# Optimization experiments

Hardware: AMD Instinct MI355X
Metric: run time of the kernel (lower is better)

## Reference

```python
import jax, jax.numpy as jnp
import numpy as np

NV, NS = 100000, 50000
EVV, EH, EIN, ESS = 1_600_000, 800_000, 800_000, 800_000
DIN, H, OUT, K, NREL = 5, 64, 8, 3, 3


def _seg_sum(x, idx, n):
    return jax.ops.segment_sum(x, idx, num_segments=n)


def _seg_mean(x, idx, n):
    s = _seg_sum(x, idx, n)
    c = _seg_sum(jnp.ones(idx.shape, x.dtype), idx, n)
    return s / jnp.maximum(c, 1.0)[:, None]


def rgcn(x, ei, etype, W_rel, W_root, b):
    # PyG RGCNConv: per-relation mean aggregation + root transform + bias
    src, dst = ei[0], ei[1]
    out = x @ W_root + b
    for r in range(NREL):
        xr = x @ W_rel[r]                    # [NV,H] transform-then-gather
        w = (etype == r).astype(x.dtype)     # [E] relation mask
        s = _seg_sum(xr[src] * w[:, None], dst, NV)
        c = _seg_sum(w, dst, NV)
        out = out + s / jnp.maximum(c, 1.0)[:, None]
    return out


def tag(x, ei, W, b, n):
    # PyG TAGConv: sym-normalized (no self loops) K-hop propagation, per-hop linear
    src, dst = ei[0], ei[1]
    deg = _seg_sum(jnp.ones(src.shape, x.dtype), dst, n)
    dinv = jnp.where(deg > 0, jax.lax.rsqrt(jnp.maximum(deg, 1.0)), 0.0)
    norm = dinv[src] * dinv[dst]             # [E]
    out = x @ W[0]
    h = x
    for k in range(1, K + 1):
        h = _seg_sum(norm[:, None] * h[src], dst, n)
        out = out + h @ W[k]
    return out + b


def graph_conv(x_src, x_dst, ei, ew, W_rel, b, W_root, n_dst):
    # PyG GraphConv (aggr='add'): lin_rel(sum_j w_ij x_j) + lin_root(x_i)
    src, dst = ei[0], ei[1]
    agg = _seg_sum(ew[:, None] * x_src[src], dst, n_dst)
    return agg @ W_rel + b + x_dst @ W_root


def sage(x_src, x_dst, ei, W_l, b, W_r, n_dst):
    # PyG SAGEConv (aggr='mean'): lin_l(mean_j x_j) + lin_r(x_i)
    src, dst = ei[0], ei[1]
    agg = _seg_mean(x_src[src], dst, n_dst)
    return agg @ W_l + b + x_dst @ W_r


def setup_inputs() -> dict:
    key = jax.random.key(0)
    ks = jax.random.split(key, 40)
    f32 = jnp.float32

    def nrm(k, shape, fan_in):
        return jax.random.normal(k, shape, f32) / np.sqrt(fan_in)

    def ei(k, e, nsrc, ndst):
        k1, k2 = jax.random.split(k)
        return jnp.stack([jax.random.randint(k1, (e,), 0, nsrc),
                          jax.random.randint(k2, (e,), 0, ndst)]).astype(jnp.int64)

    inp = {
        'game_x': jax.random.normal(ks[0], (NV, DIN), f32),
        'state_x': jax.random.normal(ks[1], (NS, DIN), f32),
        'edge_index_v_v': ei(ks[2], EVV, NV, NV),
        'edge_type_v_v': jax.random.randint(ks[3], (EVV,), 0, NREL).astype(jnp.int64),
        'edge_index_history_v_s': ei(ks[4], EH, NV, NS),
        'edge_attr_history_v_s': jax.random.uniform(ks[5], (EH,), f32),
        'edge_index_in_v_s': ei(ks[6], EIN, NV, NS),
        'edge_index_s_s': ei(ks[7], ESS, NS, NS),
        # conv1 RGCN(5,H,3)
        'W1_rel': nrm(ks[8], (NREL, DIN, H), DIN), 'W1_root': nrm(ks[9], (DIN, H), DIN), 'b1': jnp.zeros((H,), f32),
        # conv12 TAG(5,H,K=3)
        'W12': nrm(ks[10], (K + 1, DIN, H), DIN), 'b12': jnp.zeros((H,), f32),
        # conv2 TAG(H,H,K=3)
        'W2': nrm(ks[11], (K + 1, H, H), H), 'b2': jnp.zeros((H,), f32),
        # conv3 GraphConv((H,DIN)->H)
        'W3_rel': nrm(ks[12], (H, H), H), 'W3_root': nrm(ks[13], (DIN, H), DIN), 'b3': jnp.zeros((H,), f32),
        # conv32 SAGE((H,H)->H)
        'W32_l': nrm(ks[14], (H, H), H), 'W32_r': nrm(ks[15], (H, H), H), 'b32': jnp.zeros((H,), f32),
        'W4_l': nrm(ks[16], (H, H), H), 'W4_r': nrm(ks[17], (H, H), H), 'b4': jnp.zeros((H,), f32),
        'W42_l': nrm(ks[18], (H, H), H), 'W42_r': nrm(ks[19], (H, H), H), 'b42': jnp.zeros((H,), f32),
        'W5_l': nrm(ks[20], (H, H), H), 'W5_r': nrm(ks[21], (H, H), H), 'b5': jnp.zeros((H,), f32),
        'Wl': nrm(ks[22], (H, OUT), H), 'bl': jnp.zeros((OUT,), f32),
    }
    return inp


def reference(game_x, state_x, edge_index_v_v, edge_type_v_v,
              edge_index_history_v_s, edge_attr_history_v_s,
              edge_index_in_v_s, edge_index_s_s,
              W1_rel, W1_root, b1, W12, b12, W2, b2,
              W3_rel, W3_root, b3, W32_l, W32_r, b32,
              W4_l, W4_r, b4, W42_l, W42_r, b42,
              W5_l, W5_r, b5, Wl, bl):
    gx = rgcn(game_x, edge_index_v_v, edge_type_v_v, W1_rel, W1_root, b1) \
        + tag(game_x, edge_index_v_v, W12, b12, NV)          # group(..., 'sum')
    sx = jax.nn.relu(graph_conv(gx, state_x, edge_index_history_v_s,
                                edge_attr_history_v_s, W3_rel, b3, W3_root, NS))
    sx = jax.nn.relu(sage(gx, sx, edge_index_history_v_s, W32_l, b32, W32_r, NS))
    sx = jax.nn.relu(sage(gx, sx, edge_index_in_v_s, W4_l, b4, W4_r, NS))
    sx = jax.nn.relu(sage(gx, sx, edge_index_in_v_s, W42_l, b42, W42_r, NS))
    sx = jax.nn.relu(tag(sx, edge_index_s_s, W2, b2, NS))
    sx = jax.nn.relu(sage(sx, sx, edge_index_s_s, W5_l, b5, W5_r, NS))
    return sx @ Wl + bl
```

## Files before the change

kernel.cpp:

```cpp
#include <hip/hip_runtime.h>

#define NVV 100000
#define NSV 50000
#define E_VV 1600000
#define E_H  800000
#define E_IN 800000
#define E_SS 800000
#define ETOT 4000000
#define DIN 5
#define H_ROW 100000
#define IN_ROW 150000
#define SS_ROW 200000
#define NROWS 250000
#define POS_H  E_VV
#define POS_IN (E_VV + E_H)
#define POS_SS (E_VV + E_H + E_IN)
#define NBUK 196
#define NBUKS 98
#define NBTOT 490
#define BUK_H  196
#define BUK_IN 294
#define BUK_SS 392
#define BSHIFT 9
#define T1 4096
#define TC 16384
#define G1VV 391
#define G1S  196
#define SB1  (G1VV + 3 * G1S)

__device__ __forceinline__ unsigned short f2bf(float x) {
  unsigned b = __float_as_uint(x);
  return (unsigned short)((b + 0x7FFFu + ((b >> 16) & 1u)) >> 16);
}
__device__ __forceinline__ float bf2f(unsigned short u) {
  return __uint_as_float(((unsigned)u) << 16);
}


__global__ __launch_bounds__(256)
void k_bucket_count(const int* __restrict__ d_vv, const int* __restrict__ d_h,
                    const int* __restrict__ d_in, const int* __restrict__ d_ss,
                    int* __restrict__ bcnt) {
  __shared__ int h[NBTOT];
  const int tid = threadIdx.x;
  for (int i = tid; i < NBTOT; i += 256) h[i] = 0;
  __syncthreads();
  const int base = blockIdx.x * TC;
#pragma unroll 4
  for (int k = 0; k < TC / 256; k++) {
    int e = base + k * 256 + tid;
    int bi = -1;
    if (e < E_VV) bi = d_vv[e] >> BSHIFT;
    else if (e < POS_IN) bi = BUK_H + (d_h[e - POS_H] >> BSHIFT);
    else if (e < POS_SS) bi = BUK_IN + (d_in[e - POS_IN] >> BSHIFT);
    else if (e < ETOT) bi = BUK_SS + (d_ss[e - POS_SS] >> BSHIFT);
    if (bi >= 0) atomicAdd(&h[bi], 1);
  }
  __syncthreads();
  for (int i = tid; i < NBTOT; i += 256) if (h[i]) atomicAdd(&bcnt[i], h[i]);
}

__global__ __launch_bounds__(512)
void k_bucket_scan(const int* __restrict__ bcnt, int* __restrict__ bbase, int* __restrict__ cb) {
  __shared__ int sd[512];
  int t = threadIdx.x;
  int v = (t < NBTOT) ? bcnt[t] : 0;
  sd[t] = v; __syncthreads();
  for (int off = 1; off < 512; off <<= 1) {
    int x = (t >= off) ? sd[t - off] : 0;
    __syncthreads();
    sd[t] += x;
    __syncthreads();
  }
  int segstart = (t < BUK_H) ? 0 : (t < BUK_IN) ? BUK_H : (t < BUK_SS) ? BUK_IN : BUK_SS;
  int excl = ((t > 0) ? sd[t - 1] : 0) - ((segstart > 0) ? sd[segstart - 1] : 0);
  if (t < NBTOT) { bbase[t] = excl; cb[t] = excl; }
}

__global__ __launch_bounds__(256)
void k_fill_s1_all(const int* __restrict__ s_vv, const int* __restrict__ d_vv,
                   const int* __restrict__ et,
                   const int* __restrict__ s_h, const int* __restrict__ d_h,
                   const float* __restrict__ ew,
                   const int* __restrict__ s_in, const int* __restrict__ d_in,
                   const int* __restrict__ s_ss, const int* __restrict__ d_ss,
                   int* __restrict__ cb,
                   unsigned* __restrict__ temp_vv, uint2* __restrict__ temp_h,
                   unsigned* __restrict__ temp_in, unsigned* __restrict__ temp_ss) {
  __shared__ int hist[NBUK], lbase[NBUK], run[NBUK], gb[NBUK];
  __shared__ int sc[256];
  __shared__ unsigned stage[T1];
  __shared__ unsigned stageW[T1];
  __shared__ int gpos[T1];
  const int tid = threadIdx.x;
  const int b = blockIdx.x;
  int g, tile;
  if (b < G1VV) { g = 0; tile = b; }
  else if (b < G1VV + G1S) { g = 1; tile = b - G1VV; }
  else if (b < G1VV + 2 * G1S) { g = 2; tile = b - G1VV - G1S; }
  else { g = 3; tile = b - G1VV - 2 * G1S; }
  const int ne = (g == 0) ? E_VV : E_H;
  const int nbuk = (g == 0) ? NBUK : NBUKS;
  const int cboff = (g == 0) ? 0 : (g == 1) ? BUK_H : (g == 2) ? BUK_IN : BUK_SS;
  const int* S = (g == 0) ? s_vv : (g == 1) ? s_h : (g == 2) ? s_in : s_ss;
  const int* D = (g == 0) ? d_vv : (g == 1) ? d_h : (g == 2) ? d_in : d_ss;
  const int base = tile * T1;
  const int nvalid = min(T1, ne - base);
  for (int i = tid; i < nbuk; i += 256) { hist[i] = 0; run[i] = 0; }
  __syncthreads();
  int dv[16]; unsigned pk[16], pkw[16];
#pragma unroll
  for (int k = 0; k < 16; k++) {
    int e = base + k * 256 + tid;
    if (e - base < nvalid) {
      int d = D[e];
      dv[k] = d;
      if (g == 0) pk[k] = (unsigned)(((d & 511) << 19) | (et[e] << 17) | S[e]);
      else pk[k] = (unsigned)(((d & 511) << 17) | S[e]);
      if (g == 1) pkw[k] = (unsigned)__float_as_int(ew[e]);
      atomicAdd(&hist[d >> BSHIFT], 1);
    } else dv[k] = -1;
  }
  __syncthreads();
  int my = (tid < nbuk) ? hist[tid] : 0;
  sc[tid] = my; __syncthreads();
  for (int off = 1; off < 256; off <<= 1) {
    int t = (tid >= off) ? sc[tid - off] : 0;
    __syncthreads();
    sc[tid] += t;
    __syncthreads();
  }
  if (tid < nbuk) {
    lbase[tid] = sc[tid] - my;
    gb[tid] = my ? atomicAdd(&cb[cboff + tid], my) : 0;
  }
  __syncthreads();
#pragma unroll
  for (int k = 0; k < 16; k++) {
    if (dv[k] >= 0) {
      int bu = dv[k] >> BSHIFT;
      int loc = atomicAdd(&run[bu], 1);
      int li = lbase[bu] + loc;
      stage[li] = pk[k];
      if (g == 1) stageW[li] = pkw[k];
      gpos[li] = gb[bu] + loc;
    }
  }
  __syncthreads();
  if (g == 0)      for (int i = tid; i < nvalid; i += 256) temp_vv[gpos[i]] = stage[i];
  else if (g == 1) for (int i = tid; i < nvalid; i += 256) temp_h[gpos[i]] = make_uint2(stage[i], stageW[i]);
  else if (g == 2) for (int i = tid; i < nvalid; i += 256) temp_in[gpos[i]] = stage[i];
  else             for (int i = tid; i < nvalid; i += 256) temp_ss[gpos[i]] = stage[i];
}

__global__ __launch_bounds__(256)
void k_fill_s2_all(const unsigned* __restrict__ temp_vv, const uint2* __restrict__ temp_h,
                   const unsigned* __restrict__ temp_in, const unsigned* __restrict__ temp_ss,
                   const int* __restrict__ bbase,
                   unsigned* __restrict__ payload_vv, int2* __restrict__ eh,
                   int* __restrict__ srcs_in, int* __restrict__ srcs_ss,
                   int* __restrict__ rs_all, int* __restrict__ cnt_all,
                   const float* __restrict__ x, float4* __restrict__ xp,
                   float* __restrict__ dinvS) {
  __shared__ int lcnt[512], lpos[512];
  __shared__ int sc[256];
  const int b = blockIdx.x, tid = threadIdx.x;
  int g, lb;
  if (b < BUK_H) { g = 0; lb = b; }
  else if (b < BUK_IN) { g = 1; lb = b - BUK_H; }
  else if (b < BUK_SS) { g = 2; lb = b - BUK_IN; }
  else { g = 3; lb = b - BUK_SS; }
  const int d0 = lb << BSHIFT;
  const int nrows = (g == 0) ? NVV : NSV;
  const int rowbase = (g == 0) ? 0 : (g == 1) ? H_ROW : (g == 2) ? IN_ROW : SS_ROW;
  const int ne = (g == 0) ? E_VV : E_H;
  const int lastb = (g == 0) ? NBUK - 1 : NBUKS - 1;
  const int shift = (g == 0) ? 19 : 17;
  lcnt[tid] = 0; lcnt[tid + 256] = 0;
  __syncthreads();
  const int gstart = bbase[b];
  const int gend = (lb == lastb) ? ne : bbase[b + 1];
  if (g == 1) {
    for (int i = gstart + tid; i < gend; i += 256) atomicAdd(&lcnt[temp_h[i].x >> 17], 1);
  } else {
    const unsigned* tp = (g == 0) ? temp_vv : (g == 2) ? temp_in : temp_ss;
    for (int i = gstart + tid; i < gend; i += 256) atomicAdd(&lcnt[tp[i] >> shift], 1);
  }
  __syncthreads();
  int c0 = lcnt[2 * tid], c1 = lcnt[2 * tid + 1];
  int ps = c0 + c1;
  sc[tid] = ps; __syncthreads();
  for (int off = 1; off < 256; off <<= 1) {
    int x2 = (tid >= off) ? sc[tid - off] : 0;
    __syncthreads();
    sc[tid] += x2;
    __syncthreads();
  }
  int basep = gstart + sc[tid] - ps;
  lpos[2 * tid] = basep;
  lpos[2 * tid + 1] = basep + c0;
  __syncthreads();
  for (int d = tid; d < 512; d += 256) {
    int gd = d0 + d;
    if (gd < nrows) {
      rs_all[rowbase + gd] = lpos[d];
      cnt_all[rowbase + gd] = lcnt[d];
      if (g == 0) {
        float dc = (float)lcnt[d];
        float di = dc > 0.f ? rsqrtf(dc) : 0.f;
        const float* xr = x + (size_t)gd * 5;
        xp[gd * 2]     = make_float4(xr[0], xr[1], xr[2], xr[3]);
        xp[gd * 2 + 1] = make_float4(xr[4], di, 0.f, 0.f);
      } else if (g == 3) {
        float dc = (float)lcnt[d];
        dinvS[gd] = dc > 0.f ? rsqrtf(dc) : 0.f;
      }
    }
  }
  __syncthreads();
  if (g == 0) {
    for (int i = gstart + tid; i < gend; i += 256) {
      unsigned en = temp_vv[i];
      int pos = atomicAdd(&lpos[en >> 19], 1);
      payload_vv[pos] = en & 0x7FFFFu;
    }
  } else if (g == 1) {
    for (int i = gstart + tid; i < gend; i += 256) {
      uint2 en = temp_h[i];
      int pos = atomicAdd(&lpos[en.x >> 17], 1);
      eh[pos] = make_int2((int)(en.x & 0x1FFFFu), (int)en.y);
    }
  } else if (g == 2) {
    for (int i = gstart + tid; i < gend; i += 256) {
      unsigned en = temp_in[i];
      int pos = atomicAdd(&lpos[en >> 17], 1);
      srcs_in[pos] = (int)(en & 0x1FFFFu);
    }
  } else {
    for (int i = gstart + tid; i < gend; i += 256) {
      unsigned en = temp_ss[i];
      int pos = atomicAdd(&lpos[en >> 17], 1);
      srcs_ss[pos] = (int)(en & 0x1FFFFu);
    }
  }
}


__global__ __launch_bounds__(256)
void k_vv_pass1(const float4* __restrict__ xp,
                const int* __restrict__ rowstart, const int* __restrict__ cnt,
                const unsigned* __restrict__ payload,
                float4* __restrict__ ra4all, float4* __restrict__ h1p) {
  int d = blockIdx.x * 256 + threadIdx.x;
  if (d >= NVV) return;
  int rs = rowstart[d], c = cnt[d];
  float a0[5] = {0,0,0,0,0}, a1[5] = {0,0,0,0,0}, a2[5] = {0,0,0,0,0}, h[5] = {0,0,0,0,0};
  float c0 = 0.f, c1 = 0.f, c2 = 0.f;
  int j = 0;
  for (; j + 2 <= c; j += 2) {
    unsigned pA = payload[rs + j], pB = payload[rs + j + 1];
    int sA = pA & 0x1FFFF, rA = pA >> 17;
    int sB = pB & 0x1FFFF, rB = pB >> 17;
    float4 xA0 = xp[sA * 2], xA1 = xp[sA * 2 + 1];
    float4 xB0 = xp[sB * 2], xB1 = xp[sB * 2 + 1];
    float xsA[5] = {xA0.x, xA0.y, xA0.z, xA0.w, xA1.x};
    float xsB[5] = {xB0.x, xB0.y, xB0.z, xB0.w, xB1.x};
    float wA = xA1.y, wB = xB1.y;
    float mA0 = (rA == 0) ? 1.f : 0.f, mA1 = (rA == 1) ? 1.f : 0.f, mA2 = (rA == 2) ? 1.f : 0.f;
    float mB0 = (rB == 0) ? 1.f : 0.f, mB1 = (rB == 1) ? 1.f : 0.f, mB2 = (rB == 2) ? 1.f : 0.f;
    c0 += mA0 + mB0; c1 += mA1 + mB1; c2 += mA2 + mB2;
#pragma unroll
    for (int k = 0; k < 5; k++) {
      h[k] += wA * xsA[k] + wB * xsB[k];
      a0[k] += mA0 * xsA[k] + mB0 * xsB[k];
      a1[k] += mA1 * xsA[k] + mB1 * xsB[k];
      a2[k] += mA2 * xsA[k] + mB2 * xsB[k];
    }
  }
  for (; j < c; j++) {
    unsigned p = payload[rs + j];
    int s = p & 0x1FFFF, r = p >> 17;
    float4 x0 = xp[s * 2], x1 = xp[s * 2 + 1];
    float xs[5] = {x0.x, x0.y, x0.z, x0.w, x1.x};
    float wsc = x1.y;
    float m0 = (r == 0) ? 1.f : 0.f, m1 = (r == 1) ? 1.f : 0.f, m2 = (r == 2) ? 1.f : 0.f;
    c0 += m0; c1 += m1; c2 += m2;
#pragma unroll
    for (int k = 0; k < 5; k++) {
      h[k] += wsc * xs[k];
      a0[k] += m0 * xs[k]; a1[k] += m1 * xs[k]; a2[k] += m2 * xs[k];
    }
  }
  float dv = xp[d * 2 + 1].y;
  float4* ra4 = ra4all + d * 5;
  ra4[0] = make_float4(a0[0], a0[1], a0[2], a0[3]);
  ra4[1] = make_float4(a0[4], a1[0], a1[1], a1[2]);
  ra4[2] = make_float4(a1[3], a1[4], a2[0], a2[1]);
  ra4[3] = make_float4(a2[2], a2[3], a2[4], c0);
  ra4[4] = make_float4(c1, c2, 0.f, 0.f);
  h1p[d * 2]     = make_float4(dv * h[0], dv * h[1], dv * h[2], dv * h[3]);
  h1p[d * 2 + 1] = make_float4(dv * h[4], dv, 0.f, 0.f);
}

__global__ __launch_bounds__(256)
void k_vv_hop(const float4* __restrict__ hinp,
              const int* __restrict__ rowstart, const int* __restrict__ cnt,
              const unsigned* __restrict__ payload, float4* __restrict__ houtp) {
  int d = blockIdx.x * 256 + threadIdx.x;
  if (d >= NVV) return;
  int rs = rowstart[d], c = cnt[d];
  float h[5] = {0,0,0,0,0};
  int j = 0;
  for (; j + 4 <= c; j += 4) {
    unsigned p0 = payload[rs + j], p1 = payload[rs + j + 1];
    unsigned p2 = payload[rs + j + 2], p3 = payload[rs + j + 3];
    int s0 = p0 & 0x1FFFF, s1 = p1 & 0x1FFFF, s2 = p2 & 0x1FFFF, s3 = p3 & 0x1FFFF;
    float4 a0 = hinp[s0 * 2], b0 = hinp[s0 * 2 + 1];
    float4 a1 = hinp[s1 * 2], b1 = hinp[s1 * 2 + 1];
    float4 a2 = hinp[s2 * 2], b2 = hinp[s2 * 2 + 1];
    float4 a3 = hinp[s3 * 2], b3 = hinp[s3 * 2 + 1];
    float w0 = b0.y, w1 = b1.y, w2 = b2.y, w3 = b3.y;
    h[0] += w0 * a0.x + w1 * a1.x + w2 * a2.x + w3 * a3.x;
    h[1] += w0 * a0.y + w1 * a1.y + w2 * a2.y + w3 * a3.y;
    h[2] += w0 * a0.z + w1 * a1.z + w2 * a2.z + w3 * a3.z;
    h[3] += w0 * a0.w + w1 * a1.w + w2 * a2.w + w3 * a3.w;
    h[4] += w0 * b0.x + w1 * b1.x + w2 * b2.x + w3 * b3.x;
  }
  for (; j < c; j++) {
    int s = payload[rs + j] & 0x1FFFF;
    float4 x0 = hinp[s * 2], x1 = hinp[s * 2 + 1];
    float wsc = x1.y;
    h[0] += wsc * x0.x; h[1] += wsc * x0.y; h[2] += wsc * x0.z; h[3] += wsc * x0.w;
    h[4] += wsc * x1.x;
  }
  float dv = hinp[d * 2 + 1].y;
  houtp[d * 2]     = make_float4(dv * h[0], dv * h[1], dv * h[2], dv * h[3]);
  houtp[d * 2 + 1] = make_float4(dv * h[4], dv, 0.f, 0.f);
}

__global__ __launch_bounds__(256)
void k_combine_gx(const float4* __restrict__ xp,
                  const float4* __restrict__ ra4all,
                  const float4* __restrict__ h1p, const float4* __restrict__ h2p,
                  const float4* __restrict__ h3p,
                  const float* __restrict__ W1_rel, const float* __restrict__ W1_root,
                  const float* __restrict__ b1,
                  const float* __restrict__ W12, const float* __restrict__ b12,
                  unsigned short* __restrict__ gx16) {
  __shared__ float Ws[7 * 320];
  __shared__ float bs[64];
  int tid = threadIdx.x;
  for (int i = tid; i < 320; i += 256) {
    Ws[i]        = W1_root[i] + W12[i];
    Ws[320 + i]  = W1_rel[i];
    Ws[640 + i]  = W1_rel[320 + i];
    Ws[960 + i]  = W1_rel[640 + i];
    Ws[1280 + i] = W12[320 + i];
    Ws[1600 + i] = W12[640 + i];
    Ws[1920 + i] = W12[960 + i];
  }
  if (tid < 64) bs[tid] = b1[tid] + b12[tid];
  __syncthreads();
  const int f = tid & 63;
  const int grp = tid >> 6;
  float wcol[35];
#pragma unroll
  for (int t = 0; t < 35; t++) wcol[t] = Ws[t * 64 + f];
  const float bias = bs[f];
  const int v0 = blockIdx.x * 32 + grp * 8;
  for (int n = 0; n < 8; n++) {
    int v = v0 + n;
    if (v >= NVV) return;
    float in[35];
    {
      float4 x0 = xp[v * 2], x1 = xp[v * 2 + 1];
      in[0] = x0.x; in[1] = x0.y; in[2] = x0.z; in[3] = x0.w; in[4] = x1.x;
    }
    {
      const float4* ra = ra4all + v * 5;
      float4 r0 = ra[0], r1 = ra[1], r2 = ra[2], r3 = ra[3], r4 = ra[4];
      float i0 = 1.0f / fmaxf(r3.w, 1.0f);
      float i1 = 1.0f / fmaxf(r4.x, 1.0f);
      float i2 = 1.0f / fmaxf(r4.y, 1.0f);
      in[5]  = r0.x * i0; in[6]  = r0.y * i0; in[7]  = r0.z * i0; in[8]  = r0.w * i0; in[9]  = r1.x * i0;
      in[10] = r1.y * i1; in[11] = r1.z * i1; in[12] = r1.w * i1; in[13] = r2.x * i1; in[14] = r2.y * i1;
      in[15] = r2.z * i2; in[16] = r2.w * i2; in[17] = r3.x * i2; in[18] = r3.y * i2; in[19] = r3.z * i2;
    }
    {
      float4 a = h1p[v * 2], b = h1p[v * 2 + 1];
      in[20] = a.x; in[21] = a.y; in[22] = a.z; in[23] = a.w; in[24] = b.x;
      a = h2p[v * 2]; b = h2p[v * 2 + 1];
      in[25] = a.x; in[26] = a.y; in[27] = a.z; in[28] = a.w; in[29] = b.x;
      a = h3p[v * 2]; b = h3p[v * 2 + 1];
      in[30] = a.x; in[31] = a.y; in[32] = a.z; in[33] = a.w; in[34] = b.x;
    }
    float acc = bias;
#pragma unroll
    for (int t = 0; t < 35; t++) acc += in[t] * wcol[t];
    gx16[v * 64 + f] = f2bf(acc);
  }
}


__global__ __launch_bounds__(256)
void k_aggB(const unsigned short* __restrict__ X16,
            const int* __restrict__ rs_h, const int* __restrict__ cnt_h,
            const int2* __restrict__ eh,
            const int* __restrict__ rs_in, const int* __restrict__ cnt_in,
            const int* __restrict__ srcs_in,
            float* __restrict__ outw, float* __restrict__ outu, float* __restrict__ outIN,
            int nb64) {
  int bb = blockIdx.x;
  int lane = threadIdx.x & 63;
  if (bb < nb64) {
    int wid = bb * 4 + (threadIdx.x >> 6);
    if (wid >= NSV) return;
    int rs = rs_h[wid], c = cnt_h[wid];
    float aw = 0.f, au = 0.f;
    int j = 0;
    for (; j + 8 <= c; j += 8) {
      int2 p0 = eh[rs + j],     p1 = eh[rs + j + 1], p2 = eh[rs + j + 2], p3 = eh[rs + j + 3];
      int2 p4 = eh[rs + j + 4], p5 = eh[rs + j + 5], p6 = eh[rs + j + 6], p7 = eh[rs + j + 7];
      float v0 = bf2f(X16[p0.x * 64 + lane]);
      float v1 = bf2f(X16[p1.x * 64 + lane]);
      float v2 = bf2f(X16[p2.x * 64 + lane]);
      float v3 = bf2f(X16[p3.x * 64 + lane]);
      float v4 = bf2f(X16[p4.x * 64 + lane]);
      float v5 = bf2f(X16[p5.x * 64 + lane]);
      float v6 = bf2f(X16[p6.x * 64 + lane]);
      float v7 = bf2f(X16[p7.x * 64 + lane]);
      au += ((v0 + v1) + (v2 + v3)) + ((v4 + v5) + (v6 + v7));
      aw += __int_as_float(p0.y) * v0 + __int_as_float(p1.y) * v1
          + __int_as_float(p2.y) * v2 + __int_as_float(p3.y) * v3
          + __int_as_float(p4.y) * v4 + __int_as_float(p5.y) * v5
          + __int_as_float(p6.y) * v6 + __int_as_float(p7.y) * v7;
    }
    for (; j < c; j++) {
      int2 p = eh[rs + j];
      float v = bf2f(X16[p.x * 64 + lane]);
      au += v; aw += __int_as_float(p.y) * v;
    }
    outw[wid * 64 + lane] = aw;
    outu[wid * 64 + lane] = au;
  } else {
    int wid = (bb - nb64) * 4 + (threadIdx.x >> 6);
    if (wid >= NSV) return;
    int rs = rs_in[wid], c = cnt_in[wid];
    float a = 0.f;
    int j = 0;
    for (; j + 8 <= c; j += 8) {
      int s0 = srcs_in[rs + j],     s1 = srcs_in[rs + j + 1], s2 = srcs_in[rs + j + 2], s3 = srcs_in[rs + j + 3];
      int s4 = srcs_in[rs + j + 4], s5 = srcs_in[rs + j + 5], s6 = srcs_in[rs + j + 6], s7 = srcs_in[rs + j + 7];
      float v0 = bf2f(X16[s0 * 64 + lane]);
      float v1 = bf2f(X16[s1 * 64 + lane]);
      float v2 = bf2f(X16[s2 * 64 + lane]);
      float v3 = bf2f(X16[s3 * 64 + lane]);
      float v4 = bf2f(X16[s4 * 64 + lane]);
      float v5 = bf2f(X16[s5 * 64 + lane]);
      float v6 = bf2f(X16[s6 * 64 + lane]);
      float v7 = bf2f(X16[s7 * 64 + lane]);
      a += ((v0 + v1) + (v2 + v3)) + ((v4 + v5) + (v6 + v7));
    }
    for (; j < c; j++) a += bf2f(X16[srcs_in[rs + j] * 64 + lane]);
    outIN[wid * 64 + lane] = a;
  }
}

__global__ __launch_bounds__(256)
void k_agg64b(const unsigned short* __restrict__ X16,
              const int* __restrict__ rowstart, const int* __restrict__ cnt,
              const int* __restrict__ srcs, float* __restrict__ out, int n) {
  int wid = blockIdx.x * 4 + (threadIdx.x >> 6);
  if (wid >= n) return;
  int lane = threadIdx.x & 63;
  int rs = rowstart[wid], c = cnt[wid];
  float a = 0.f;
  int j = 0;
  for (; j + 8 <= c; j += 8) {
    int s0 = srcs[rs + j],     s1 = srcs[rs + j + 1], s2 = srcs[rs + j + 2], s3 = srcs[rs + j + 3];
    int s4 = srcs[rs + j + 4], s5 = srcs[rs + j + 5], s6 = srcs[rs + j + 6], s7 = srcs[rs + j + 7];
    float v0 = bf2f(X16[s0 * 64 + lane]);
    float v1 = bf2f(X16[s1 * 64 + lane]);
    float v2 = bf2f(X16[s2 * 64 + lane]);
    float v3 = bf2f(X16[s3 * 64 + lane]);
    float v4 = bf2f(X16[s4 * 64 + lane]);
    float v5 = bf2f(X16[s5 * 64 + lane]);
    float v6 = bf2f(X16[s6 * 64 + lane]);
    float v7 = bf2f(X16[s7 * 64 + lane]);
    a += ((v0 + v1) + (v2 + v3)) + ((v4 + v5) + (v6 + v7));
  }
  for (; j < c; j++) a += bf2f(X16[srcs[rs + j] * 64 + lane]);
  out[wid * 64 + lane] = a;
}

__global__ __launch_bounds__(256)
void k_tag64b(const unsigned short* __restrict__ U16,
              const int* __restrict__ rowstart, const int* __restrict__ cnt,
              const int* __restrict__ srcs, const float* __restrict__ dinv,
              unsigned short* __restrict__ t_out, unsigned short* __restrict__ u_out, int n) {
  int wid = blockIdx.x * 4 + (threadIdx.x >> 6);
  if (wid >= n) return;
  int lane = threadIdx.x & 63;
  int rs = rowstart[wid], c = cnt[wid];
  float a = 0.f;
  int j = 0;
  for (; j + 8 <= c; j += 8) {
    int s0 = srcs[rs + j],     s1 = srcs[rs + j + 1], s2 = srcs[rs + j + 2], s3 = srcs[rs + j + 3];
    int s4 = srcs[rs + j + 4], s5 = srcs[rs + j + 5], s6 = srcs[rs + j + 6], s7 = srcs[rs + j + 7];
    float v0 = bf2f(U16[s0 * 64 + lane]);
    float v1 = bf2f(U16[s1 * 64 + lane]);
    float v2 = bf2f(U16[s2 * 64 + lane]);
    float v3 = bf2f(U16[s3 * 64 + lane]);
    float v4 = bf2f(U16[s4 * 64 + lane]);
    float v5 = bf2f(U16[s5 * 64 + lane]);
    float v6 = bf2f(U16[s6 * 64 + lane]);
    float v7 = bf2f(U16[s7 * 64 + lane]);
    a += ((v0 + v1) + (v2 + v3)) + ((v4 + v5) + (v6 + v7));
  }
  for (; j < c; j++) a += bf2f(U16[srcs[rs + j] * 64 + lane]);
  float dv = dinv[wid];
  float t = dv * a;
  t_out[wid * 64 + lane] = f2bf(t);
  if (u_out) u_out[wid * 64 + lane] = f2bf(dv * t);
}


__device__ __forceinline__ void mm_zero(float acc[4][4]) {
#pragma unroll
  for (int j = 0; j < 4; j++)
#pragma unroll
    for (int jj = 0; jj < 4; jj++) acc[j][jj] = 0.f;
}

__device__ __forceinline__ void mm_acc(const float* sA, const float* sW, int K,
                                       int nl0, int f0, float acc[4][4]) {
  for (int k = 0; k < K; k++) {
    float4 w = *(const float4*)(&sW[k * 64 + f0]);
#pragma unroll
    for (int j = 0; j < 4; j++) {
      float a = sA[(nl0 + j) * 68 + k];
      acc[j][0] += a * w.x; acc[j][1] += a * w.y; acc[j][2] += a * w.z; acc[j][3] += a * w.w;
    }
  }
}

__device__ __forceinline__ void mm_loadw(float* Ws, const float* W, int tid) {
  const float4* w4 = (const float4*)W;
  float4* s4 = (float4*)Ws;
  for (int i = tid; i < 1024; i += 256) s4[i] = w4[i];
}

__device__ __forceinline__ void mm_stage_f32(float* as, const float* A, const int* cntA,
                                             int gb, int n, int tid) {
  for (int i = tid; i < 1024; i += 256) {
    int nl = i >> 4, k4 = i & 15;
    int g = gb + nl;
    float4 v = make_float4(0.f, 0.f, 0.f, 0.f);
    if (g < n) {
      v = ((const float4*)A)[g * 16 + k4];
      if (cntA) {
        float sc = 1.0f / fmaxf((float)cntA[g], 1.0f);
        v.x *= sc; v.y *= sc; v.z *= sc; v.w *= sc;
      }
    }
    *(float4*)(&as[nl * 68 + k4 * 4]) = v;
  }
}

__device__ __forceinline__ void mm_stage_bf16(float* as, const unsigned short* A,
                                              int gb, int n, int tid) {
  for (int i = tid; i < 1024; i += 256) {
    int nl = i >> 4, k4 = i & 15;
    int g = gb + nl;
    float4 v = make_float4(0.f, 0.f, 0.f, 0.f);
    if (g < n) {
      uint2 u = ((const uint2*)(A + (size_t)g * 64))[k4];
      v.x = bf2f((unsigned short)(u.x & 0xFFFF));
      v.y = bf2f((unsigned short)(u.x >> 16));
      v.z = bf2f((unsigned short)(u.y & 0xFFFF));
      v.w = bf2f((unsigned short)(u.y >> 16));
    }
    *(float4*)(&as[nl * 68 + k4 * 4]) = v;
  }
}

__global__ __launch_bounds__(256)
void k_mm_chainC(const float* __restrict__ aggHw, const float* __restrict__ state_x,
                 const float* __restrict__ aggHu, const int* __restrict__ cnt_h,
                 const float* __restrict__ aggIN, const int* __restrict__ cnt_in,
                 const float* __restrict__ W3_rel, const float* __restrict__ W3_root,
                 const float* __restrict__ b3,
                 const float* __restrict__ W32_l, const float* __restrict__ W32_r,
                 const float* __restrict__ b32,
                 const float* __restrict__ W4_l, const float* __restrict__ W4_r,
                 const float* __restrict__ b4,
                 const float* __restrict__ W42_l, const float* __restrict__ W42_r,
                 const float* __restrict__ b42,
                 float* __restrict__ S2out, unsigned short* __restrict__ S2b,
                 const float* __restrict__ dinvS, int n) {
  __shared__ float Ws[4096];
  __shared__ float as[64 * 68];
  __shared__ float cs[64 * 68];
  const int tid = threadIdx.x;
  const int gb = blockIdx.x * 64;
  const int lane = tid & 63;
  const int fq = lane & 15, nq = lane >> 4;
  const int f0 = fq * 4;
  const int nl0 = (tid >> 6) * 16 + nq * 4;
  float acc[4][4];

  mm_loadw(Ws, W3_rel, tid);
  mm_stage_f32(as, aggHw, nullptr, gb, n, tid);
  __syncthreads();
  mm_zero(acc);
  mm_acc(as, Ws, 64, nl0, f0, acc);
  __syncthreads();
  for (int i = tid; i < 320; i += 256) {
    int nl = i / 5, k = i - nl * 5;
    int g = gb + nl;
    as[nl * 68 + k] = (g < n) ? state_x[(size_t)g * 5 + k] : 0.f;
  }
  for (int i = tid; i < 320; i += 256) Ws[i] = W3_root[i];
  __syncthreads();
  mm_acc(as, Ws, 5, nl0, f0, acc);
#pragma unroll
  for (int j = 0; j < 4; j++)
#pragma unroll
    for (int jj = 0; jj < 4; jj++)
      cs[(nl0 + j) * 68 + f0 + jj] = fmaxf(acc[j][jj] + b3[f0 + jj], 0.f);
  __syncthreads();

  mm_loadw(Ws, W32_l, tid);
  mm_stage_f32(as, aggHu, cnt_h, gb, n, tid);
  __syncthreads();
  mm_zero(acc);
  mm_acc(as, Ws, 64, nl0, f0, acc);
  __syncthreads();
  mm_loadw(Ws, W32_r, tid);
  __syncthreads();
  mm_acc(cs, Ws, 64, nl0, f0, acc);
  __syncthreads();
#pragma unroll
  for (int j = 0; j < 4; j++)
#pragma unroll
    for (int jj = 0; jj < 4; jj++)
      cs[(nl0 + j) * 68 + f0 + jj] = fmaxf(acc[j][jj] + b32[f0 + jj], 0.f);
  __syncthreads();

  mm_loadw(Ws, W4_l, tid);
  mm_stage_f32(as, aggIN, cnt_in, gb, n, tid);
  __syncthreads();
  mm_zero(acc);
  mm_acc(as, Ws, 64, nl0, f0, acc);
  __syncthreads();
  mm_loadw(Ws, W4_r, tid);
  __syncthreads();
  mm_acc(cs, Ws, 64, nl0, f0, acc);
  __syncthreads();
#pragma unroll
  for (int j = 0; j < 4; j++)
#pragma unroll
    for (int jj = 0; jj < 4; jj++)
      cs[(nl0 + j) * 68 + f0 + jj] = fmaxf(acc[j][jj] + b4[f0 + jj], 0.f);
  __syncthreads();

  mm_loadw(Ws, W42_l, tid);
  mm_stage_f32(as, aggIN, cnt_in, gb, n, tid);
  __syncthreads();
  mm_zero(acc);
  mm_acc(as, Ws, 64, nl0, f0, acc);
  __syncthreads();
  mm_loadw(Ws, W42_r, tid);
  __syncthreads();
  mm_acc(cs, Ws, 64, nl0, f0, acc);
#pragma unroll
  for (int j = 0; j < 4; j++) {
    int g = gb + nl0 + j;
    if (g < n) {
      float osc = dinvS[g];
#pragma unroll
      for (int jj = 0; jj < 4; jj++) {
        int f = f0 + jj;
        float v = fmaxf(acc[j][jj] + b42[f], 0.f);
        S2out[(size_t)g * 64 + f] = v;
        S2b[(size_t)g * 64 + f] = f2bf(v * osc);
      }
    }
  }
}

__global__ __launch_bounds__(256)
void k_mm_d(const float* __restrict__ S2, const unsigned short* __restrict__ t1b,
            const unsigned short* __restrict__ t2b, const unsigned short* __restrict__ t3b,
            const float* __restrict__ W2, const float* __restrict__ b2,
            float* __restrict__ S1, unsigned short* __restrict__ S1b, int n) {
  __shared__ float Ws[4096];
  __shared__ float as[64 * 68];
  const int tid = threadIdx.x;
  const int gb = blockIdx.x * 64;
  const int lane = tid & 63;
  const int fq = lane & 15, nq = lane >> 4;
  const int f0 = fq * 4;
  const int nl0 = (tid >> 6) * 16 + nq * 4;
  float acc[4][4];
  mm_zero(acc);
  mm_loadw(Ws, W2, tid);
  mm_stage_f32(as, S2, nullptr, gb, n, tid);
  __syncthreads();
  mm_acc(as, Ws, 64, nl0, f0, acc);
  __syncthreads();
  mm_loadw(Ws, W2 + 4096, tid);
  mm_stage_bf16(as, t1b, gb, n, tid);
  __syncthreads();
  mm_acc(as, Ws, 64, nl0, f0, acc);
  __syncthreads();
  mm_loadw(Ws, W2 + 8192, tid);
  mm_stage_bf16(as, t2b, gb, n, tid);
  __syncthreads();
  mm_acc(as, Ws, 64, nl0, f0, acc);
  __syncthreads();
  mm_loadw(Ws, W2 + 12288, tid);
  mm_stage_bf16(as, t3b, gb, n, tid);
  __syncthreads();
  mm_acc(as, Ws, 64, nl0, f0, acc);
#pragma unroll
  for (int j = 0; j < 4; j++) {
    int g = gb + nl0 + j;
    if (g < n) {
#pragma unroll
      for (int jj = 0; jj < 4; jj++) {
        int f = f0 + jj;
        float v = fmaxf(acc[j][jj] + b2[f], 0.f);
        S1[(size_t)g * 64 + f] = v;
        S1b[(size_t)g * 64 + f] = f2bf(v);
      }
    }
  }
}

__global__ __launch_bounds__(256)
void k_mm_e(const float* __restrict__ aggSS, const int* __restrict__ cnt_ss,
            const float* __restrict__ W5_l, const float* __restrict__ S1,
            const float* __restrict__ W5_r, const float* __restrict__ b5,
            const float* __restrict__ Wl, const float* __restrict__ bl,
            float* __restrict__ out, int n) {
  __shared__ float Ws[4096];
  __shared__ float as[64 * 68];
  __shared__ float cs[64 * 68];
  const int tid = threadIdx.x;
  const int gb = blockIdx.x * 64;
  const int lane = tid & 63;
  const int fq = lane & 15, nq = lane >> 4;
  const int f0 = fq * 4;
  const int nl0 = (tid >> 6) * 16 + nq * 4;
  float acc[4][4];
  mm_zero(acc);
  mm_loadw(Ws, W5_l, tid);
  mm_stage_f32(as, aggSS, cnt_ss, gb, n, tid);
  __syncthreads();
  mm_acc(as, Ws, 64, nl0, f0, acc);
  __syncthreads();
  mm_loadw(Ws, W5_r, tid);
  mm_stage_f32(cs, S1, nullptr, gb, n, tid);
  __syncthreads();
  mm_acc(cs, Ws, 64, nl0, f0, acc);
  __syncthreads();
#pragma unroll
  for (int j = 0; j < 4; j++)
#pragma unroll
    for (int jj = 0; jj < 4; jj++)
      as[(nl0 + j) * 68 + f0 + jj] = fmaxf(acc[j][jj] + b5[f0 + jj], 0.f);
  for (int i = tid; i < 512; i += 256) Ws[i] = Wl[i];
  __syncthreads();
#pragma unroll
  for (int q = 0; q < 2; q++) {
    int idx = tid * 2 + q;
    int nl = idx >> 3, o = idx & 7;
    int g = gb + nl;
    if (g < n) {
      float a2 = bl[o];
#pragma unroll 8
      for (int k = 0; k < 64; k++) a2 += as[nl * 68 + k] * Ws[k * 8 + o];
      out[(size_t)g * 8 + o] = a2;
    }
  }
}


extern "C" void kernel_launch(void* const* d_in, const int* in_sizes, int n_in,
                              void* d_out, int out_size, void* d_ws, size_t ws_size,
                              hipStream_t stream) {
  const float* game_x  = (const float*)d_in[0];
  const float* state_x = (const float*)d_in[1];
  const int*   ei_vv   = (const int*)d_in[2];
  const int*   et_vv   = (const int*)d_in[3];
  const int*   ei_h    = (const int*)d_in[4];
  const float* ew_h    = (const float*)d_in[5];
  const int*   ei_in   = (const int*)d_in[6];
  const int*   ei_ss   = (const int*)d_in[7];
  const float* W1_rel  = (const float*)d_in[8];
  const float* W1_root = (const float*)d_in[9];
  const float* b1      = (const float*)d_in[10];
  const float* W12     = (const float*)d_in[11];
  const float* b12     = (const float*)d_in[12];
  const float* W2      = (const float*)d_in[13];
  const float* b2      = (const float*)d_in[14];
  const float* W3_rel  = (const float*)d_in[15];
  const float* W3_root = (const float*)d_in[16];
  const float* b3      = (const float*)d_in[17];
  const float* W32_l   = (const float*)d_in[18];
  const float* W32_r   = (const float*)d_in[19];
  const float* b32     = (const float*)d_in[20];
  const float* W4_l    = (const float*)d_in[21];
  const float* W4_r    = (const float*)d_in[22];
  const float* b4      = (const float*)d_in[23];
  const float* W42_l   = (const float*)d_in[24];
  const float* W42_r   = (const float*)d_in[25];
  const float* b42     = (const float*)d_in[26];
  const float* W5_l    = (const float*)d_in[27];
  const float* W5_r    = (const float*)d_in[28];
  const float* b5      = (const float*)d_in[29];
  const float* Wl      = (const float*)d_in[30];
  const float* bl      = (const float*)d_in[31];

  float* ws = (float*)d_ws;
  int*   cnt_all = (int*)(ws + 0);
  int*   rs_all  = (int*)(ws + 250000);
  int*   bcnt    = (int*)(ws + 500000);
  int*   bbase   = (int*)(ws + 500512);
  int*   cb      = (int*)(ws + 501024);
  int*   srcs_ss = (int*)(ws + 760000);
  float4* x_pad  = (float4*)(ws + 1600000);
  float4* h1p    = (float4*)(ws + 2400000);
  float4* h2p    = (float4*)(ws + 3200000);
  float4* h3p    = (float4*)(ws + 4000000);
  float4* ra4all = (float4*)(ws + 4800000);
  float* dinvS   = ws + 6800000;
  unsigned short* gx16 = (unsigned short*)(ws + 6850000);
  unsigned* temp_vv    = (unsigned*)(ws + 6850000);
  float* aggHw = ws + 10050000;
  float* aggHu = ws + 13250000;
  float* aggIN = ws + 16450000;
  float* S1    = ws + 19650000;
  float* S2    = ws + 22850000;
  uint2*    temp_h  = (uint2*)aggHw;
  unsigned* temp_in = (unsigned*)(aggHw + 1600000);
  unsigned* temp_ss = (unsigned*)(aggHw + 2400000);
  unsigned short* S2b = (unsigned short*)(ws + 4800000);
  unsigned short* u1b = (unsigned short*)(aggHw + 1600000);
  float*          aggSS = aggHw + 1600000;
  unsigned short* t1b = (unsigned short*)aggHu;
  unsigned short* t2b = (unsigned short*)(aggHu + 1600000);
  unsigned short* t3b = (unsigned short*)aggIN;
  unsigned short* S1b = (unsigned short*)(aggIN + 1600000);
  unsigned* payload_vv = (unsigned*)S1;
  unsigned short* u2b  = (unsigned short*)S1;
  int2*     eh         = (int2*)S2;
  int*      srcs_in    = (int*)(S2 + 1600000);

  const int* src_vv = ei_vv;  const int* dst_vv = ei_vv + E_VV;
  const int* src_h  = ei_h;   const int* dst_h  = ei_h + E_H;
  const int* src_in = ei_in;  const int* dst_in = ei_in + E_IN;
  const int* src_ss = ei_ss;  const int* dst_ss = ei_ss + E_SS;

  auto nblk = [](long long n) { return dim3((unsigned)((n + 255) / 256)); };
  const int NB64 = (NSV + 3) / 4;
  const int NB   = (NSV + 63) / 64;
  const int GC   = (ETOT + TC - 1) / TC;

  int* cnt_h  = cnt_all + H_ROW;
  int* cnt_in = cnt_all + IN_ROW;
  int* cnt_ss = cnt_all + SS_ROW;
  int* rs_vv  = rs_all;
  int* rs_h   = rs_all + H_ROW;
  int* rs_in  = rs_all + IN_ROW;
  int* rs_ss  = rs_all + SS_ROW;

  hipMemsetAsync(bcnt, 0, NBTOT * sizeof(int), stream);
  k_bucket_count<<<GC, 256, 0, stream>>>(dst_vv, dst_h, dst_in, dst_ss, bcnt);
  k_bucket_scan<<<1, 512, 0, stream>>>(bcnt, bbase, cb);
  k_fill_s1_all<<<SB1, 256, 0, stream>>>(src_vv, dst_vv, et_vv, src_h, dst_h, ew_h,
                                         src_in, dst_in, src_ss, dst_ss, cb,
                                         temp_vv, temp_h, temp_in, temp_ss);
  k_fill_s2_all<<<NBTOT, 256, 0, stream>>>(temp_vv, temp_h, temp_in, temp_ss, bbase,
                                           payload_vv, eh, srcs_in, srcs_ss,
                                           rs_all, cnt_all, game_x, x_pad, dinvS);

  k_vv_pass1<<<nblk(NVV), 256, 0, stream>>>(x_pad, rs_vv, cnt_all, payload_vv, ra4all, h1p);
  k_vv_hop<<<nblk(NVV), 256, 0, stream>>>(h1p, rs_vv, cnt_all, payload_vv, h2p);
  k_vv_hop<<<nblk(NVV), 256, 0, stream>>>(h2p, rs_vv, cnt_all, payload_vv, h3p);
  k_combine_gx<<<dim3((NVV + 31) / 32), 256, 0, stream>>>(x_pad, ra4all, h1p, h2p, h3p,
                                                          W1_rel, W1_root, b1, W12, b12, gx16);

  k_aggB<<<2 * NB64, 256, 0, stream>>>(gx16, rs_h, cnt_h, eh, rs_in, cnt_in, srcs_in,
                                       aggHw, aggHu, aggIN, NB64);

  k_mm_chainC<<<NB, 256, 0, stream>>>(aggHw, state_x, aggHu, cnt_h, aggIN, cnt_in,
                                      W3_rel, W3_root, b3, W32_l, W32_r, b32,
                                      W4_l, W4_r, b4, W42_l, W42_r, b42,
                                      S2, S2b, dinvS, NSV);

  k_tag64b<<<NB64, 256, 0, stream>>>(S2b, rs_ss, cnt_ss, srcs_ss, dinvS, t1b, u1b, NSV);
  k_tag64b<<<NB64, 256, 0, stream>>>(u1b, rs_ss, cnt_ss, srcs_ss, dinvS, t2b, u2b, NSV);
  k_tag64b<<<NB64, 256, 0, stream>>>(u2b, rs_ss, cnt_ss, srcs_ss, dinvS, t3b, nullptr, NSV);
  k_mm_d<<<NB, 256, 0, stream>>>(S2, t1b, t2b, t3b, W2, b2, S1, S1b, NSV);

  k_agg64b<<<NB64, 256, 0, stream>>>(S1b, rs_ss, cnt_ss, srcs_ss, aggSS, NSV);
  k_mm_e<<<NB, 256, 0, stream>>>(aggSS, cnt_ss, W5_l, S1, W5_r, b5, Wl, bl, (float*)d_out, NSV);
}
```

Before: 683.4 us.

## Software-pipeline weight and activation loads into registers in dense matmul kernels

Splits the shared-memory staging of weights and activation tiles into a register issue phase and a commit phase. The next stage's global loads are issued before the current matmul runs, so their latency overlaps compute. Biases, root weights, state features and dinv scales are also hoisted into registers at kernel start. This removes one barrier per layer, but raises register pressure from the extra float4 buffers, which could lower occupancy.

```diff
diff --git a/kernel.cpp b/kernel.cpp
--- a/kernel.cpp
+++ b/kernel.cpp
@@ -544,42 +544,65 @@
   }
 }
 
-__device__ __forceinline__ void mm_loadw(float* Ws, const float* W, int tid) {
+__device__ __forceinline__ void wq_issue(const float* __restrict__ W, int tid, float4 r[4]) {
   const float4* w4 = (const float4*)W;
+#pragma unroll
+  for (int i = 0; i < 4; i++) r[i] = w4[tid + i * 256];
+}
+__device__ __forceinline__ void wq_commit(float* Ws, int tid, const float4 r[4]) {
   float4* s4 = (float4*)Ws;
-  for (int i = tid; i < 1024; i += 256) s4[i] = w4[i];
-}
-
-__device__ __forceinline__ void mm_stage_f32(float* as, const float* A, const int* cntA,
-                                             int gb, int n, int tid) {
-  for (int i = tid; i < 1024; i += 256) {
-    int nl = i >> 4, k4 = i & 15;
+#pragma unroll
+  for (int i = 0; i < 4; i++) s4[tid + i * 256] = r[i];
+}
+__device__ __forceinline__ void aq_issue_f32(const float* __restrict__ A,
+                                             const int* __restrict__ cntA,
+                                             int gb, int n, int tid,
+                                             float4 r[4], float cn[4]) {
+#pragma unroll
+  for (int i = 0; i < 4; i++) {
+    int idx = tid + i * 256;
+    int nl = idx >> 4, k4 = idx & 15;
     int g = gb + nl;
-    float4 v = make_float4(0.f, 0.f, 0.f, 0.f);
-    if (g < n) {
-      v = ((const float4*)A)[g * 16 + k4];
-      if (cntA) {
-        float sc = 1.0f / fmaxf((float)cntA[g], 1.0f);
-        v.x *= sc; v.y *= sc; v.z *= sc; v.w *= sc;
-      }
+    bool ok = g < n;
+    r[i] = ok ? ((const float4*)A)[g * 16 + k4] : make_float4(0.f, 0.f, 0.f, 0.f);
+    cn[i] = (cntA && ok) ? (float)cntA[g] : 1.f;
+  }
+}
+__device__ __forceinline__ void aq_commit_f32(float* as, int tid, bool scaled,
+                                              const float4 r[4], const float cn[4]) {
+#pragma unroll
+  for (int i = 0; i < 4; i++) {
+    int idx = tid + i * 256;
+    int nl = idx >> 4, k4 = idx & 15;
+    float4 v = r[i];
+    if (scaled) {
+      float sc = 1.0f / fmaxf(cn[i], 1.0f);
+      v.x *= sc; v.y *= sc; v.z *= sc; v.w *= sc;
     }
     *(float4*)(&as[nl * 68 + k4 * 4]) = v;
   }
 }
-
-__device__ __forceinline__ void mm_stage_bf16(float* as, const unsigned short* A,
-                                              int gb, int n, int tid) {
-  for (int i = tid; i < 1024; i += 256) {
-    int nl = i >> 4, k4 = i & 15;
+__device__ __forceinline__ void aq_issue_bf16(const unsigned short* __restrict__ A,
+                                              int gb, int n, int tid, uint2 r[4]) {
+#pragma unroll
+  for (int i = 0; i < 4; i++) {
+    int idx = tid + i * 256;
+    int nl = idx >> 4, k4 = idx & 15;
     int g = gb + nl;
-    float4 v = make_float4(0.f, 0.f, 0.f, 0.f);
-    if (g < n) {
-      uint2 u = ((const uint2*)(A + (size_t)g * 64))[k4];
-      v.x = bf2f((unsigned short)(u.x & 0xFFFF));
-      v.y = bf2f((unsigned short)(u.x >> 16));
-      v.z = bf2f((unsigned short)(u.y & 0xFFFF));
-      v.w = bf2f((unsigned short)(u.y >> 16));
-    }
+    r[i] = (g < n) ? ((const uint2*)(A + (size_t)g * 64))[k4] : make_uint2(0u, 0u);
+  }
+}
+__device__ __forceinline__ void aq_commit_bf16(float* as, int tid, const uint2 r[4]) {
+#pragma unroll
+  for (int i = 0; i < 4; i++) {
+    int idx = tid + i * 256;
+    int nl = idx >> 4, k4 = idx & 15;
+    uint2 u = r[i];
+    float4 v;
+    v.x = bf2f((unsigned short)(u.x & 0xFFFF));
+    v.y = bf2f((unsigned short)(u.x >> 16));
+    v.z = bf2f((unsigned short)(u.y & 0xFFFF));
+    v.w = bf2f((unsigned short)(u.y >> 16));
     *(float4*)(&as[nl * 68 + k4 * 4]) = v;
   }
 }
@@ -608,82 +631,116 @@
   const int f0 = fq * 4;
   const int nl0 = (tid >> 6) * 16 + nq * 4;
   float acc[4][4];
-
-  mm_loadw(Ws, W3_rel, tid);
-  mm_stage_f32(as, aggHw, nullptr, gb, n, tid);
+  float4 pW[4], qW[4], pA[4], qA[4];
+  float pC[4], qC[4];
+
+  wq_issue(W3_rel, tid, pW);
+  aq_issue_f32(aggHw, nullptr, gb, n, tid, pA, pC);
+  float rt0 = W3_root[tid];
+  float rt1 = (tid < 64) ? W3_root[256 + tid] : 0.f;
+  const int nlA = tid / 5, kA = tid - nlA * 5;
+  float sxA = (gb + nlA < n) ? state_x[(size_t)(gb + nlA) * 5 + kA] : 0.f;
+  const int iB = tid + 256;
+  const int nlB = iB / 5, kB = iB - nlB * 5;
+  float sxB = (tid < 64 && gb + nlB < n) ? state_x[(size_t)(gb + nlB) * 5 + kB] : 0.f;
+  float4 rb3  = ((const float4*)b3)[fq];
+  float4 rb32 = ((const float4*)b32)[fq];
+  float4 rb4  = ((const float4*)b4)[fq];
+  float4 rb42 = ((const float4*)b42)[fq];
+  float rdv[4];
+#pragma unroll
+  for (int j = 0; j < 4; j++) {
+    int g = gb + nl0 + j;
+    rdv[j] = (g < n) ? dinvS[g] : 0.f;
+  }
+  wq_issue(W32_l, tid, qW);
+  aq_issue_f32(aggHu, cnt_h, gb, n, tid, qA, qC);
+
+  wq_commit(Ws, tid, pW);
+  aq_commit_f32(as, tid, false, pA, pC);
   __syncthreads();
   mm_zero(acc);
   mm_acc(as, Ws, 64, nl0, f0, acc);
   __syncthreads();
-  for (int i = tid; i < 320; i += 256) {
-    int nl = i / 5, k = i - nl * 5;
-    int g = gb + nl;
-    as[nl * 68 + k] = (g < n) ? state_x[(size_t)g * 5 + k] : 0.f;
-  }
-  for (int i = tid; i < 320; i += 256) Ws[i] = W3_root[i];
+  Ws[tid] = rt0;
+  if (tid < 64) Ws[256 + tid] = rt1;
+  as[nlA * 68 + kA] = sxA;
+  if (tid < 64) as[nlB * 68 + kB] = sxB;
   __syncthreads();
   mm_acc(as, Ws, 5, nl0, f0, acc);
-#pragma unroll
-  for (int j = 0; j < 4; j++)
-#pragma unroll
-    for (int jj = 0; jj < 4; jj++)
-      cs[(nl0 + j) * 68 + f0 + jj] = fmaxf(acc[j][jj] + b3[f0 + jj], 0.f);
-  __syncthreads();
-
-  mm_loadw(Ws, W32_l, tid);
-  mm_stage_f32(as, aggHu, cnt_h, gb, n, tid);
+  {
+    float bb[4] = {rb3.x, rb3.y, rb3.z, rb3.w};
+#pragma unroll
+    for (int j = 0; j < 4; j++)
+#pragma unroll
+      for (int jj = 0; jj < 4; jj++)
+        cs[(nl0 + j) * 68 + f0 + jj] = fmaxf(acc[j][jj] + bb[jj], 0.f);
+  }
+  __syncthreads();
+  wq_commit(Ws, tid, qW);
+  aq_commit_f32(as, tid, true, qA, qC);
+  wq_issue(W32_r, tid, pW);
   __syncthreads();
   mm_zero(acc);
   mm_acc(as, Ws, 64, nl0, f0, acc);
   __syncthreads();
-  mm_loadw(Ws, W32_r, tid);
+  wq_commit(Ws, tid, pW);
+  wq_issue(W4_l, tid, qW);
+  aq_issue_f32(aggIN, cnt_in, gb, n, tid, qA, qC);
   __syncthreads();
   mm_acc(cs, Ws, 64, nl0, f0, acc);
   __syncthreads();
-#pragma unroll
-  for (int j = 0; j < 4; j++)
-#pragma unroll
-    for (int jj = 0; jj < 4; jj++)
-      cs[(nl0 + j) * 68 + f0 + jj] = fmaxf(acc[j][jj] + b32[f0 + jj], 0.f);
-  __syncthreads();
-
-  mm_loadw(Ws, W4_l, tid);
-  mm_stage_f32(as, aggIN, cnt_in, gb, n, tid);
+  {
+    float bb[4] = {rb32.x, rb32.y, rb32.z, rb32.w};
+#pragma unroll
+    for (int j = 0; j < 4; j++)
+#pragma unroll
+      for (int jj = 0; jj < 4; jj++)
+        cs[(nl0 + j) * 68 + f0 + jj] = fmaxf(acc[j][jj] + bb[jj], 0.f);
+  }
+  wq_commit(Ws, tid, qW);
+  aq_commit_f32(as, tid, true, qA, qC);
+  wq_issue(W4_r, tid, pW);
   __syncthreads();
   mm_zero(acc);
   mm_acc(as, Ws, 64, nl0, f0, acc);
   __syncthreads();
-  mm_loadw(Ws, W4_r, tid);
+  wq_commit(Ws, tid, pW);
+  wq_issue(W42_l, tid, qW);
   __syncthreads();
   mm_acc(cs, Ws, 64, nl0, f0, acc);
   __syncthreads();
-#pragma unroll
-  for (int j = 0; j < 4; j++)
-#pragma unroll
-    for (int jj = 0; jj < 4; jj++)
-      cs[(nl0 + j) * 68 + f0 + jj] = fmaxf(acc[j][jj] + b4[f0 + jj], 0.f);
-  __syncthreads();
-
-  mm_loadw(Ws, W42_l, tid);
-  mm_stage_f32(as, aggIN, cnt_in, gb, n, tid);
+  {
+    float bb[4] = {rb4.x, rb4.y, rb4.z, rb4.w};
+#pragma unroll
+    for (int j = 0; j < 4; j++)
+#pragma unroll
+      for (int jj = 0; jj < 4; jj++)
+        cs[(nl0 + j) * 68 + f0 + jj] = fmaxf(acc[j][jj] + bb[jj], 0.f);
+  }
+  wq_commit(Ws, tid, qW);
+  wq_issue(W42_r, tid, pW);
   __syncthreads();
   mm_zero(acc);
   mm_acc(as, Ws, 64, nl0, f0, acc);
   __syncthreads();
-  mm_loadw(Ws, W42_r, tid);
+  wq_commit(Ws, tid, pW);
   __syncthreads();
   mm_acc(cs, Ws, 64, nl0, f0, acc);
-#pragma unroll
-  for (int j = 0; j < 4; j++) {
-    int g = gb + nl0 + j;
-    if (g < n) {
-      float osc = dinvS[g];
-#pragma unroll
-      for (int jj = 0; jj < 4; jj++) {
-        int f = f0 + jj;
-        float v = fmaxf(acc[j][jj] + b42[f], 0.f);
-        S2out[(size_t)g * 64 + f] = v;
-        S2b[(size_t)g * 64 + f] = f2bf(v * osc);
+  {
+    float bb[4] = {rb42.x, rb42.y, rb42.z, rb42.w};
+#pragma unroll
+    for (int j = 0; j < 4; j++) {
+      int g = gb + nl0 + j;
+      if (g < n) {
+        float osc = rdv[j];
+#pragma unroll
+        for (int jj = 0; jj < 4; jj++) {
+          int f = f0 + jj;
+          float v = fmaxf(acc[j][jj] + bb[jj], 0.f);
+          S2out[(size_t)g * 64 + f] = v;
+          S2b[(size_t)g * 64 + f] = f2bf(v * osc);
+        }
       }
     }
   }
@@ -703,36 +760,53 @@
   const int f0 = fq * 4;
   const int nl0 = (tid >> 6) * 16 + nq * 4;
   float acc[4][4];
+  float4 pW[4], qW[4], pA[4];
+  float pC[4];
+  uint2 pB[4], qB[4];
+
+  wq_issue(W2, tid, pW);
+  aq_issue_f32(S2, nullptr, gb, n, tid, pA, pC);
+  wq_issue(W2 + 4096, tid, qW);
+  aq_issue_bf16(t1b, gb, n, tid, qB);
+  float4 rb2 = ((const float4*)b2)[fq];
+
+  wq_commit(Ws, tid, pW);
+  aq_commit_f32(as, tid, false, pA, pC);
+  __syncthreads();
   mm_zero(acc);
-  mm_loadw(Ws, W2, tid);
-  mm_stage_f32(as, S2, nullptr, gb, n, tid);
-  __syncthreads();
   mm_acc(as, Ws, 64, nl0, f0, acc);
   __syncthreads();
-  mm_loadw(Ws, W2 + 4096, tid);
-  mm_stage_bf16(as, t1b, gb, n, tid);
+  wq_commit(Ws, tid, qW);
+  aq_commit_bf16(as, tid, qB);
+  wq_issue(W2 + 8192, tid, pW);
+  aq_issue_bf16(t2b, gb, n, tid, pB);
   __syncthreads();
   mm_acc(as, Ws, 64, nl0, f0, acc);
   __syncthreads();
-  mm_loadw(Ws, W2 + 8192, tid);
-  mm_stage_bf16(as, t2b, gb, n, tid);
+  wq_commit(Ws, tid, pW);
+  aq_commit_bf16(as, tid, pB);
+  wq_issue(W2 + 12288, tid, qW);
+  aq_issue_bf16(t3b, gb, n, tid, qB);
   __syncthreads();
   mm_acc(as, Ws, 64, nl0, f0, acc);
   __syncthreads();
-  mm_loadw(Ws, W2 + 12288, tid);
-  mm_stage_bf16(as, t3b, gb, n, tid);
+  wq_commit(Ws, tid, qW);
+  aq_commit_bf16(as, tid, qB);
   __syncthreads();
   mm_acc(as, Ws, 64, nl0, f0, acc);
-#pragma unroll
-  for (int j = 0; j < 4; j++) {
-    int g = gb + nl0 + j;
-    if (g < n) {
-#pragma unroll
-      for (int jj = 0; jj < 4; jj++) {
-        int f = f0 + jj;
-        float v = fmaxf(acc[j][jj] + b2[f], 0.f);
-        S1[(size_t)g * 64 + f] = v;
-        S1b[(size_t)g * 64 + f] = f2bf(v);
+  {
+    float bb[4] = {rb2.x, rb2.y, rb2.z, rb2.w};
+#pragma unroll
+    for (int j = 0; j < 4; j++) {
+      int g = gb + nl0 + j;
+      if (g < n) {
+#pragma unroll
+        for (int jj = 0; jj < 4; jj++) {
+          int f = f0 + jj;
+          float v = fmaxf(acc[j][jj] + bb[jj], 0.f);
+          S1[(size_t)g * 64 + f] = v;
+          S1b[(size_t)g * 64 + f] = f2bf(v);
+        }
       }
     }
   }
@@ -754,23 +828,40 @@
   const int f0 = fq * 4;
   const int nl0 = (tid >> 6) * 16 + nq * 4;
   float acc[4][4];
+  float4 pW[4], qW[4], pA[4], qA[4];
+  float pC[4], qC[4];
+
+  wq_issue(W5_l, tid, pW);
+  aq_issue_f32(aggSS, cnt_ss, gb, n, tid, pA, pC);
+  wq_issue(W5_r, tid, qW);
+  aq_issue_f32(S1, nullptr, gb, n, tid, qA, qC);
+  float rwl0 = Wl[tid];
+  float rwl1 = Wl[256 + tid];
+  float4 rb5 = ((const float4*)b5)[fq];
+  float rbl0 = bl[(2 * tid) & 7];
+  float rbl1 = bl[(2 * tid + 1) & 7];
+
+  wq_commit(Ws, tid, pW);
+  aq_commit_f32(as, tid, true, pA, pC);
+  __syncthreads();
   mm_zero(acc);
-  mm_loadw(Ws, W5_l, tid);
-  mm_stage_f32(as, aggSS, cnt_ss, gb, n, tid);
-  __syncthreads();
   mm_acc(as, Ws, 64, nl0, f0, acc);
   __syncthreads();
-  mm_loadw(Ws, W5_r, tid);
-  mm_stage_f32(cs, S1, nullptr, gb, n, tid);
+  wq_commit(Ws, tid, qW);
+  aq_commit_f32(cs, tid, false, qA, qC);
   __syncthreads();
   mm_acc(cs, Ws, 64, nl0, f0, acc);
   __syncthreads();
-#pragma unroll
-  for (int j = 0; j < 4; j++)
-#pragma unroll
-    for (int jj = 0; jj < 4; jj++)
-      as[(nl0 + j) * 68 + f0 + jj] = fmaxf(acc[j][jj] + b5[f0 + jj], 0.f);
-  for (int i = tid; i < 512; i += 256) Ws[i] = Wl[i];
+  {
+    float bb[4] = {rb5.x, rb5.y, rb5.z, rb5.w};
+#pragma unroll
+    for (int j = 0; j < 4; j++)
+#pragma unroll
+      for (int jj = 0; jj < 4; jj++)
+        as[(nl0 + j) * 68 + f0 + jj] = fmaxf(acc[j][jj] + bb[jj], 0.f);
+  }
+  Ws[tid] = rwl0;
+  Ws[256 + tid] = rwl1;
   __syncthreads();
 #pragma unroll
   for (int q = 0; q < 2; q++) {
@@ -778,7 +869,7 @@
     int nl = idx >> 3, o = idx & 7;
     int g = gb + nl;
     if (g < n) {
-      float a2 = bl[o];
+      float a2 = (q == 0) ? rbl0 : rbl1;
 #pragma unroll 8
       for (int k = 0; k < 64; k++) a2 += as[nl * 68 + k] * Ws[k * 8 + o];
       out[(size_t)g * 8 + o] = a2;
```

Result: no change. 688.5 us (+0.8%).
